# Optimization experiments

Hardware: AMD Instinct MI355X
Metric: run time of the kernel (lower is better)

The kernel has to match this reference:

```python
import jax, jax.numpy as jnp
import numpy as np

HEADS = 4
DIM_HEAD = 32
GROUPS = 32  # min(256//4, 32)
EPS = 1e-5


def setup_inputs() -> dict:
    key = jax.random.key(0)
    ks = jax.random.split(key, 6)
    B, C, H, W = 16, 256, 64, 64
    hidden = HEADS * DIM_HEAD  # 128
    return {
        "x": jax.random.normal(ks[0], (B, C, H, W), dtype=jnp.float32),
        "gn_w": jax.random.uniform(ks[1], (C,), dtype=jnp.float32),
        "gn_b": jax.random.normal(ks[2], (C,), dtype=jnp.float32) * 0.05,
        "qkv_w": jax.random.normal(ks[3], (3 * hidden, C), dtype=jnp.float32) * 0.05,
        "qkv_b": jax.random.normal(ks[4], (3 * hidden,), dtype=jnp.float32) * 0.05,
        "out_w": jax.random.normal(ks[5], (C, hidden), dtype=jnp.float32) * 0.05,
        "out_b": jnp.zeros((C,), dtype=jnp.float32),
    }


def _forward_single(x, gn_w, gn_b, qkv_w, qkv_b, out_w, out_b):
    # x: (c, h, w)
    c, h, w = x.shape
    # GroupNorm over (channels-in-group, h, w)
    xg = x.reshape(GROUPS, c // GROUPS, h, w)
    mean = xg.mean(axis=(1, 2, 3), keepdims=True)
    var = xg.var(axis=(1, 2, 3), keepdims=True)
    xn = ((xg - mean) * jax.lax.rsqrt(var + EPS)).reshape(c, h, w)
    xn = xn * gn_w[:, None, None] + gn_b[:, None, None]
    # 1x1 conv QKV projection
    qkv = jnp.einsum('oc,chw->ohw', qkv_w, xn) + qkv_b[:, None, None]
    qkv = qkv.reshape(3, HEADS, DIM_HEAD, h * w)
    q, k, v = qkv[0], qkv[1], qkv[2]
    k = jax.nn.softmax(k, axis=-1)  # softmax over spatial
    context = jnp.einsum('hdn,hen->hde', k, v)   # (heads, d, d)
    out = jnp.einsum('hde,hdn->hen', context, q)  # (heads, d, n)
    out = out.reshape(HEADS * DIM_HEAD, h, w)
    # 1x1 conv output projection
    return jnp.einsum('oc,chw->ohw', out_w, out) + out_b[:, None, None]


def reference(x, gn_w, gn_b, qkv_w, qkv_b, out_w, out_b):
    f = lambda xi: _forward_single(xi, gn_w, gn_b, qkv_w, qkv_b, out_w, out_b)
    return jax.vmap(f)(x)
```

## Files before the change

kernel.cpp:

```cpp
#include <hip/hip_runtime.h>
#include <stdint.h>

typedef unsigned short u16;
typedef __attribute__((ext_vector_type(8))) short bf16x8;
typedef __attribute__((ext_vector_type(4))) float f32x4;

#define B_   16
#define C_   256
#define HW_  4096
#define QR_  384
#define HID_ 128

__device__ __forceinline__ float b2f(u16 u) {
  union { uint32_t i; float f; } v; v.i = ((uint32_t)u) << 16; return v.f;
}
__device__ __forceinline__ u16 f2b(float f) {
  union { float f; uint32_t i; } v; v.f = f;
  uint32_t r = (v.i + 0x7FFFu + ((v.i >> 16) & 1u)) >> 16;
  return (u16)r;
}

__global__ __launch_bounds__(256) void gn_stats_conv_kernel(
    const float* __restrict__ x, const float* __restrict__ gnw,
    const float* __restrict__ gnb, float* __restrict__ scale,
    float* __restrict__ shiftv,
    const float* __restrict__ qkvw, u16* __restrict__ cqkvw,
    u16* __restrict__ wqT)
{
  if (blockIdx.x >= 512) {
    int bi = blockIdx.x - 512;
    int t = threadIdx.x;
    if (bi < 96) {
      int i = bi * 256 + t;
      float4 f = ((const float4*)qkvw)[i];
      ushort4 o;
      o.x = f2b(f.x); o.y = f2b(f.y); o.z = f2b(f.z); o.w = f2b(f.w);
      ((ushort4*)cqkvw)[i] = o;
      return;
    }
    __shared__ u16 tl[16][272];
    for (int j = 0; j < 8; ++j) {
      int d = j * 16 + (t >> 4);
      int cb = (t & 15) * 16;
#pragma unroll
      for (int ii = 0; ii < 16; ++ii)
        tl[t >> 4][cb + ii] = f2b(qkvw[(size_t)d * 256 + cb + ii]);
      __syncthreads();
      union { u16 v[16]; uint4 q[2]; } pk;
#pragma unroll
      for (int dd = 0; dd < 16; ++dd) pk.v[dd] = tl[dd][t];
      *(uint4*)(wqT + (size_t)t * 128 + j * 16)     = pk.q[0];
      *(uint4*)(wqT + (size_t)t * 128 + j * 16 + 8) = pk.q[1];
      __syncthreads();
    }
    return;
  }
  int b = blockIdx.x >> 5, g = blockIdx.x & 31;
  const float* p = x + ((size_t)b * C_ + g * 8) * HW_;
  int t = threadIdx.x;
  float s = 0.f, sq = 0.f;
#pragma unroll
  for (int i = 0; i < 16; ++i) {
    float4 u0 = *(const float4*)(p + t * 8 + i * 2048);
    float4 u1 = *(const float4*)(p + t * 8 + i * 2048 + 4);
    s  += u0.x + u0.y + u0.z + u0.w + u1.x + u1.y + u1.z + u1.w;
    sq += u0.x*u0.x + u0.y*u0.y + u0.z*u0.z + u0.w*u0.w
        + u1.x*u1.x + u1.y*u1.y + u1.z*u1.z + u1.w*u1.w;
  }
#pragma unroll
  for (int off = 32; off > 0; off >>= 1) {
    s  += __shfl_down(s, off);
    sq += __shfl_down(sq, off);
  }
  __shared__ float ps[4], pq[4], mr[2];
  int lane = t & 63, w = t >> 6;
  if (lane == 0) { ps[w] = s; pq[w] = sq; }
  __syncthreads();
  if (t == 0) {
    float S = ps[0] + ps[1] + ps[2] + ps[3];
    float Q = pq[0] + pq[1] + pq[2] + pq[3];
    float mean = S * (1.f / 32768.f);
    float var  = Q * (1.f / 32768.f) - mean * mean;
    mr[0] = mean; mr[1] = rsqrtf(var + 1e-5f);
  }
  __syncthreads();
  if (t < 8) {
    int c = g * 8 + t;
    float sc = gnw[c] * mr[1];
    scale[b * C_ + c]  = sc;
    shiftv[b * C_ + c] = gnb[c] - mr[0] * sc;
  }
}

__global__ __launch_bounds__(256) void gn_transpose_kernel(
    const float* __restrict__ x, u16* __restrict__ dst,
    const float* __restrict__ scale, const float* __restrict__ shiftv)
{
  int nt = blockIdx.x, ct = blockIdx.y, b = blockIdx.z;
  const float* S = x + (size_t)b * C_ * HW_;
  u16* D = dst + (size_t)b * HW_ * C_;
  __shared__ __align__(16) u16 tile[64][136];
  int t = threadIdx.x;
  int n0 = nt * 128, c0 = ct * 64;
  int r = t >> 2, seg = (t & 3) * 32;
  float sc = scale[(size_t)b * C_ + c0 + r];
  float sh = shiftv[(size_t)b * C_ + c0 + r];
#pragma unroll
  for (int i = 0; i < 4; ++i) {
    const float* rp = S + (size_t)(c0 + r) * HW_ + n0 + seg + i * 8;
    float4 u0 = *(const float4*)(rp);
    float4 u1 = *(const float4*)(rp + 4);
    float f[8] = {u0.x, u0.y, u0.z, u0.w, u1.x, u1.y, u1.z, u1.w};
    uint4 o;
    uint32_t* op = (uint32_t*)&o;
#pragma unroll
    for (int j = 0; j < 4; ++j) {
      op[j] = (uint32_t)f2b(f[2 * j] * sc + sh)
            | ((uint32_t)f2b(f[2 * j + 1] * sc + sh) << 16);
    }
    *(uint4*)&tile[r][seg + i * 8] = o;
  }
  __syncthreads();
#pragma unroll
  for (int i = 0; i < 4; ++i) {
    int m = t * 4 + i;
    int n_l = m >> 3, cg = (m & 7) * 8;
    union { u16 v[8]; uint4 q; } pk;
#pragma unroll
    for (int e = 0; e < 8; ++e) pk.v[e] = tile[cg + e][n_l];
    *(uint4*)(D + (size_t)(n0 + n_l) * C_ + c0 + cg) = pk.q;
  }
}

__global__ __launch_bounds__(512) void kv_ctx_kernel(
    const u16* __restrict__ A,
    const u16* __restrict__ Bt,
    float* __restrict__ ctx_part,
    float* __restrict__ s_part)
{
  const int K = C_;
  int nt = blockIdx.x, b = blockIdx.y;
  const u16* Ab = A;
  const u16* Bb = Bt + (size_t)b * HW_ * C_ + (size_t)nt * 128 * K;
  __shared__ __align__(16) union {
    struct { u16 lA[256 * 64]; u16 lB[128 * 64]; } st;
    struct { u16 ek[128][136]; u16 vv[128][136]; float sred[2][128]; } ep;
    float cred[4096];
  } sm;
  int t = threadIdx.x;
  int lane = t & 63, w = t >> 6;
  int quad = lane >> 4, l16 = lane & 15;
  int wm = (w >> 1) * 64, wn = (w & 1) * 64;
  f32x4 acc[4][4];
#pragma unroll
  for (int i = 0; i < 4; ++i)
#pragma unroll
    for (int j = 0; j < 4; ++j)
#pragma unroll
      for (int r = 0; r < 4; ++r) acc[i][j][r] = 0.f;

  for (int k0 = 0; k0 < K; k0 += 64) {
    __syncthreads();
#pragma unroll
    for (int q = 0; q < 4; ++q) {
      int ch = q * 512 + t;
      int row = ch >> 3, off = (ch & 7) * 8;
      __builtin_amdgcn_global_load_lds(
          (const __attribute__((address_space(1))) void*)(Ab + (size_t)row * K + k0 + off),
          (__attribute__((address_space(3))) void*)(sm.st.lA + ch * 8), 16, 0, 0);
    }
#pragma unroll
    for (int q = 0; q < 2; ++q) {
      int ch = q * 512 + t;
      int row = ch >> 3, off = (ch & 7) * 8;
      __builtin_amdgcn_global_load_lds(
          (const __attribute__((address_space(1))) void*)(Bb + (size_t)row * K + k0 + off),
          (__attribute__((address_space(3))) void*)(sm.st.lB + ch * 8), 16, 0, 0);
    }
    __syncthreads();
    const bf16x8* A8 = (const bf16x8*)sm.st.lA;
    const bf16x8* B8 = (const bf16x8*)sm.st.lB;
#pragma unroll
    for (int kk = 0; kk < 2; ++kk) {
      bf16x8 af[4], bfr[4];
#pragma unroll
      for (int i = 0; i < 4; ++i) af[i]  = A8[(wm + i * 16 + l16) * 8 + kk * 4 + quad];
#pragma unroll
      for (int j = 0; j < 4; ++j) bfr[j] = B8[(wn + j * 16 + l16) * 8 + kk * 4 + quad];
#pragma unroll
      for (int i = 0; i < 4; ++i)
#pragma unroll
        for (int j = 0; j < 4; ++j)
          acc[i][j] = __builtin_amdgcn_mfma_f32_16x16x32_bf16(af[i], bfr[j],
                                                              acc[i][j], 0, 0, 0);
    }
  }

  __syncthreads();
  int h = w >> 1, nh = w & 1;
  if (w < 4) {
    float sl[4][4];
#pragma unroll
    for (int i = 0; i < 4; ++i)
#pragma unroll
      for (int r = 0; r < 4; ++r) sl[i][r] = 0.f;
#pragma unroll
    for (int i = 0; i < 4; ++i)
#pragma unroll
      for (int j = 0; j < 4; ++j)
#pragma unroll
        for (int r = 0; r < 4; ++r) {
          float e = __expf(acc[i][j][r]);
          sl[i][r] += e;
          sm.ep.ek[wm + i * 16 + quad * 4 + r][wn + j * 16 + l16] = f2b(e);
        }
#pragma unroll
    for (int i = 0; i < 4; ++i)
#pragma unroll
      for (int r = 0; r < 4; ++r) {
        float v = sl[i][r];
        v += __shfl_xor(v, 1);
        v += __shfl_xor(v, 2);
        v += __shfl_xor(v, 4);
        v += __shfl_xor(v, 8);
        if (l16 == 0) sm.ep.sred[nh][wm + i * 16 + quad * 4 + r] = v;
      }
  } else {
#pragma unroll
    for (int i = 0; i < 4; ++i)
#pragma unroll
      for (int j = 0; j < 4; ++j)
#pragma unroll
        for (int r = 0; r < 4; ++r)
          sm.ep.vv[wm - 128 + i * 16 + quad * 4 + r][wn + j * 16 + l16] =
              f2b(acc[i][j][r]);
  }
  __syncthreads();
  if (t < 128)
    s_part[((size_t)b * 32 + nt) * 128 + t] = sm.ep.sred[0][t] + sm.ep.sred[1][t];

  f32x4 c2[2][2];
#pragma unroll
  for (int i = 0; i < 2; ++i)
#pragma unroll
    for (int j = 0; j < 2; ++j)
#pragma unroll
      for (int r = 0; r < 4; ++r) c2[i][j][r] = 0.f;
#pragma unroll
  for (int kk = 0; kk < 2; ++kk) {
    bf16x8 ae[2], be[2];
#pragma unroll
    for (int i = 0; i < 2; ++i)
      ae[i] = *(const bf16x8*)&sm.ep.ek[h * 32 + i * 16 + l16][nh * 64 + kk * 32 + quad * 8];
#pragma unroll
    for (int j = 0; j < 2; ++j)
      be[j] = *(const bf16x8*)&sm.ep.vv[h * 32 + j * 16 + l16][nh * 64 + kk * 32 + quad * 8];
#pragma unroll
    for (int i = 0; i < 2; ++i)
#pragma unroll
      for (int j = 0; j < 2; ++j)
        c2[i][j] = __builtin_amdgcn_mfma_f32_16x16x32_bf16(ae[i], be[j], c2[i][j], 0, 0, 0);
  }
  __syncthreads();
  if (nh == 0) {
#pragma unroll
    for (int i = 0; i < 2; ++i)
#pragma unroll
      for (int j = 0; j < 2; ++j)
#pragma unroll
        for (int r = 0; r < 4; ++r)
          sm.cred[h * 1024 + (i * 16 + quad * 4 + r) * 32 + j * 16 + l16] = c2[i][j][r];
  }
  __syncthreads();
  if (nh == 1) {
#pragma unroll
    for (int i = 0; i < 2; ++i)
#pragma unroll
      for (int j = 0; j < 2; ++j)
#pragma unroll
        for (int r = 0; r < 4; ++r)
          sm.cred[h * 1024 + (i * 16 + quad * 4 + r) * 32 + j * 16 + l16] += c2[i][j][r];
  }
  __syncthreads();
  float4* dst = (float4*)(ctx_part + ((size_t)b * 32 + nt) * 4096);
  const float4* src4 = (const float4*)sm.cred;
  dst[t] = src4[t];
  dst[t + 512] = src4[t + 512];
}

__global__ __launch_bounds__(256) void fold_kernel(
    const float* __restrict__ ctx_part, const float* __restrict__ s_part,
    const float* __restrict__ outw, const float* __restrict__ qkvb,
    u16* __restrict__ wf, float* __restrict__ btp)
{
  int b = blockIdx.x >> 2, h = blockIdx.x & 3;
  int t = threadIdx.x;
  __shared__ float cs[1024];
  __shared__ float sinv[32];
  const float* cp = ctx_part + ((size_t)b * 32) * 4096 + h * 1024;
  float4 aa = make_float4(0.f, 0.f, 0.f, 0.f);
  for (int ntb = 0; ntb < 32; ++ntb) {
    float4 v = *(const float4*)(cp + (size_t)ntb * 4096 + t * 4);
    aa.x += v.x; aa.y += v.y; aa.z += v.z; aa.w += v.w;
  }
  *(float4*)&cs[t * 4] = aa;
  if (t < 32) {
    float ssum = 0.f;
    for (int ntb = 0; ntb < 32; ++ntb)
      ssum += s_part[((size_t)b * 32 + ntb) * 128 + h * 32 + t];
    sinv[t] = 1.f / ssum;
  }
  __syncthreads();
  int o = t;
  const float* wr = outw + (size_t)o * HID_ + h * 32;
  float wv[32];
  float cb = 0.f;
#pragma unroll
  for (int e = 0; e < 32; ++e) {
    wv[e] = wr[e];
    cb += wv[e] * qkvb[256 + h * 32 + e];
  }
  union { u16 v[32]; uint4 q[4]; } pk;
  float bacc = 0.f;
#pragma unroll
  for (int d = 0; d < 32; ++d) {
    float a = 0.f;
#pragma unroll
    for (int e = 0; e < 32; ++e) a += wv[e] * cs[d * 32 + e];
    float val = a * sinv[d] + cb;
    pk.v[d] = f2b(val);
    bacc += val * qkvb[h * 32 + d];
  }
  uint4* dp = (uint4*)(wf + ((size_t)b * C_ + o) * HID_ + h * 32);
#pragma unroll
  for (int i = 0; i < 4; ++i) dp[i] = pk.q[i];
  btp[((size_t)b * 4 + h) * 256 + o] = bacc;
}

__global__ __launch_bounds__(256) void wtot_gemm_kernel(
    const u16* __restrict__ wfp, const u16* __restrict__ wqT,
    u16* __restrict__ wtot)
{
  const int K = HID_;
  int nt = blockIdx.x, mt = blockIdx.y, b = blockIdx.z;
  const u16* Ab = wfp + (size_t)b * C_ * HID_ + (size_t)mt * 128 * K;
  const u16* Bb = wqT + (size_t)nt * 128 * K;
  __shared__ __align__(16) u16 lA[128 * 64];
  __shared__ __align__(16) u16 lB[128 * 64];
  int t = threadIdx.x;
  int lane = t & 63, w = t >> 6;
  int quad = lane >> 4, l16 = lane & 15;
  int wm = (w >> 1) * 64, wn = (w & 1) * 64;
  f32x4 acc[4][4];
#pragma unroll
  for (int i = 0; i < 4; ++i)
#pragma unroll
    for (int j = 0; j < 4; ++j)
#pragma unroll
      for (int r = 0; r < 4; ++r) acc[i][j][r] = 0.f;

  for (int k0 = 0; k0 < K; k0 += 64) {
    __syncthreads();
#pragma unroll
    for (int q = 0; q < 4; ++q) {
      int ch = q * 256 + t;
      int row = ch >> 3, off = (ch & 7) * 8;
      __builtin_amdgcn_global_load_lds(
          (const __attribute__((address_space(1))) void*)(Ab + (size_t)row * K + k0 + off),
          (__attribute__((address_space(3))) void*)(lA + ch * 8), 16, 0, 0);
      __builtin_amdgcn_global_load_lds(
          (const __attribute__((address_space(1))) void*)(Bb + (size_t)row * K + k0 + off),
          (__attribute__((address_space(3))) void*)(lB + ch * 8), 16, 0, 0);
    }
    __syncthreads();
    const bf16x8* A8 = (const bf16x8*)lA;
    const bf16x8* B8 = (const bf16x8*)lB;
#pragma unroll
    for (int kk = 0; kk < 2; ++kk) {
      bf16x8 af[4], bfr[4];
#pragma unroll
      for (int i = 0; i < 4; ++i) af[i]  = A8[(wm + i * 16 + l16) * 8 + kk * 4 + quad];
#pragma unroll
      for (int j = 0; j < 4; ++j) bfr[j] = B8[(wn + j * 16 + l16) * 8 + kk * 4 + quad];
#pragma unroll
      for (int i = 0; i < 4; ++i)
#pragma unroll
        for (int j = 0; j < 4; ++j)
          acc[i][j] = __builtin_amdgcn_mfma_f32_16x16x32_bf16(af[i], bfr[j],
                                                              acc[i][j], 0, 0, 0);
    }
  }
  u16* Wb = wtot + (size_t)b * C_ * C_;
#pragma unroll
  for (int i = 0; i < 4; ++i) {
#pragma unroll
    for (int rg = 0; rg < 4; ++rg) {
      int o = mt * 128 + wm + i * 16 + quad * 4 + rg;
#pragma unroll
      for (int j = 0; j < 4; ++j) {
        int c = nt * 128 + wn + j * 16 + l16;
        Wb[(size_t)o * C_ + c] = f2b(acc[i][j][rg]);
      }
    }
  }
}

__global__ __launch_bounds__(256) void out_gemm_kernel(
    const u16* __restrict__ wtot, const u16* __restrict__ Bt,
    const float* __restrict__ outb, const float* __restrict__ btp,
    float* __restrict__ Cout)
{
  const int K = C_;
  int nt = blockIdx.x, mt = blockIdx.y, b = blockIdx.z;
  const u16* Ab = wtot + (size_t)b * C_ * C_ + (size_t)mt * 128 * K;
  const u16* Bb = Bt + (size_t)b * HW_ * C_ + (size_t)nt * 128 * K;
  __shared__ __align__(16) u16 lA[128 * 64];
  __shared__ __align__(16) u16 lB[128 * 64];
  int t = threadIdx.x;
  int lane = t & 63, w = t >> 6;
  int quad = lane >> 4, l16 = lane & 15;
  int wm = (w >> 1) * 64, wn = (w & 1) * 64;
  f32x4 acc[4][4];
#pragma unroll
  for (int i = 0; i < 4; ++i)
#pragma unroll
    for (int j = 0; j < 4; ++j)
#pragma unroll
      for (int r = 0; r < 4; ++r) acc[i][j][r] = 0.f;

  for (int k0 = 0; k0 < K; k0 += 64) {
    __syncthreads();
#pragma unroll
    for (int q = 0; q < 4; ++q) {
      int ch = q * 256 + t;
      int row = ch >> 3, off = (ch & 7) * 8;
      __builtin_amdgcn_global_load_lds(
          (const __attribute__((address_space(1))) void*)(Ab + (size_t)row * K + k0 + off),
          (__attribute__((address_space(3))) void*)(lA + ch * 8), 16, 0, 0);
      __builtin_amdgcn_global_load_lds(
          (const __attribute__((address_space(1))) void*)(Bb + (size_t)row * K + k0 + off),
          (__attribute__((address_space(3))) void*)(lB + ch * 8), 16, 0, 0);
    }
    __syncthreads();
    const bf16x8* A8 = (const bf16x8*)lA;
    const bf16x8* B8 = (const bf16x8*)lB;
#pragma unroll
    for (int kk = 0; kk < 2; ++kk) {
      bf16x8 af[4], bfr[4];
#pragma unroll
      for (int i = 0; i < 4; ++i) af[i]  = A8[(wm + i * 16 + l16) * 8 + kk * 4 + quad];
#pragma unroll
      for (int j = 0; j < 4; ++j) bfr[j] = B8[(wn + j * 16 + l16) * 8 + kk * 4 + quad];
#pragma unroll
      for (int i = 0; i < 4; ++i)
#pragma unroll
        for (int j = 0; j < 4; ++j)
          acc[i][j] = __builtin_amdgcn_mfma_f32_16x16x32_bf16(af[i], bfr[j],
                                                              acc[i][j], 0, 0, 0);
    }
  }
#pragma unroll
  for (int i = 0; i < 4; ++i) {
#pragma unroll
    for (int rg = 0; rg < 4; ++rg) {
      int o = mt * 128 + wm + i * 16 + quad * 4 + rg;
      float bsv = outb[o]
                + btp[((size_t)b * 4 + 0) * 256 + o]
                + btp[((size_t)b * 4 + 1) * 256 + o]
                + btp[((size_t)b * 4 + 2) * 256 + o]
                + btp[((size_t)b * 4 + 3) * 256 + o];
      size_t rowbase = (size_t)b * C_ * HW_ + (size_t)o * HW_;
#pragma unroll
      for (int j = 0; j < 4; ++j) {
        int n = nt * 128 + wn + j * 16 + l16;
        Cout[rowbase + n] = acc[i][j][rg] + bsv;
      }
    }
  }
}

extern "C" void kernel_launch(void* const* d_in, const int* in_sizes, int n_in,
                              void* d_out, int out_size, void* d_ws, size_t ws_size,
                              hipStream_t stream)
{
  const float* x    = (const float*)d_in[0];
  const float* gnw  = (const float*)d_in[1];
  const float* gnb  = (const float*)d_in[2];
  const float* qkvw = (const float*)d_in[3];
  const float* qkvb = (const float*)d_in[4];
  const float* outw = (const float*)d_in[5];
  const float* outb = (const float*)d_in[6];

  char* p = (char*)d_ws;
  float* scale  = (float*)p;            p += (size_t)B_ * C_ * 4;
  float* shiftv = (float*)p;            p += (size_t)B_ * C_ * 4;
  u16* cqkvw = (u16*)p;                 p += (size_t)QR_ * C_ * 2;
  u16* wqT   = (u16*)p;                 p += (size_t)C_ * HID_ * 2;
  u16* xn_t  = (u16*)p;                 p += (size_t)B_ * HW_ * C_ * 2;
  u16* wf    = (u16*)p;                 p += (size_t)B_ * C_ * HID_ * 2;
  u16* wtot  = (u16*)p;                 p += (size_t)B_ * C_ * C_ * 2;
  float* ctxp = (float*)p;              p += (size_t)B_ * 32 * 4 * 1024 * 4;
  float* sp   = (float*)p;              p += (size_t)B_ * 32 * 128 * 4;
  float* btp  = (float*)p;

  gn_stats_conv_kernel<<<609, 256, 0, stream>>>(x, gnw, gnb, scale, shiftv,
                                                qkvw, cqkvw, wqT);
  gn_transpose_kernel<<<dim3(32, 4, 16), 256, 0, stream>>>(x, xn_t, scale, shiftv);
  kv_ctx_kernel<<<dim3(32, 16), 512, 0, stream>>>(cqkvw + 128 * C_, xn_t, ctxp, sp);
  fold_kernel<<<64, 256, 0, stream>>>(ctxp, sp, outw, qkvb, wf, btp);
  wtot_gemm_kernel<<<dim3(2, 2, 16), 256, 0, stream>>>(wf, wqT, wtot);
  out_gemm_kernel<<<dim3(32, 2, 16), 256, 0, stream>>>(wtot, xn_t, outb, btp,
                                                       (float*)d_out);
}
```

Measured before the change: 195.1 us.

## Fuse fold and wtot GEMM via last-block atomic counter; vectorize output stores

The separate wtot GEMM kernel is merged into the fold kernel. The last of the four head-blocks per batch, detected with an atomic counter and threadfence, stages the folded weights in LDS, computes the combined bias and the 256x256 wtot product with MFMA, and writes packed bf16. This removes one kernel launch and the btp partial-bias round trip. The output GEMM swaps its MFMA operand order so that each lane holds four consecutive spatial outputs and can write them as float4. The cost is that only 16 blocks do the wtot work, so that step runs with little parallelism.

```diff
diff --git a/kernel.cpp b/kernel.cpp
--- a/kernel.cpp
+++ b/kernel.cpp
@@ -25,7 +25,7 @@
     const float* __restrict__ gnb, float* __restrict__ scale,
     float* __restrict__ shiftv,
     const float* __restrict__ qkvw, u16* __restrict__ cqkvw,
-    u16* __restrict__ wqT)
+    u16* __restrict__ wqT, unsigned int* __restrict__ cnt)
 {
   if (blockIdx.x >= 512) {
     int bi = blockIdx.x - 512;
@@ -38,6 +38,7 @@
       ((ushort4*)cqkvw)[i] = o;
       return;
     }
+    if (t < 16) cnt[t] = 0;
     __shared__ u16 tl[16][272];
     for (int j = 0; j < 8; ++j) {
       int d = j * 16 + (t >> 4);
@@ -288,15 +289,19 @@
   dst[t + 512] = src4[t + 512];
 }
 
-__global__ __launch_bounds__(256) void fold_kernel(
+__global__ __launch_bounds__(256) void foldwtot_kernel(
     const float* __restrict__ ctx_part, const float* __restrict__ s_part,
     const float* __restrict__ outw, const float* __restrict__ qkvb,
-    u16* __restrict__ wf, float* __restrict__ btp)
+    const u16* __restrict__ wqT, const float* __restrict__ outb,
+    u16* __restrict__ wf, u16* __restrict__ wtot,
+    float* __restrict__ btot, unsigned int* __restrict__ cnt)
 {
   int b = blockIdx.x >> 2, h = blockIdx.x & 3;
   int t = threadIdx.x;
   __shared__ float cs[1024];
   __shared__ float sinv[32];
+  __shared__ unsigned int oldc;
+  __shared__ __align__(16) u16 wfl[256 * 136];
   const float* cp = ctx_part + ((size_t)b * 32) * 4096 + h * 1024;
   float4 aa = make_float4(0.f, 0.f, 0.f, 0.f);
   for (int ntb = 0; ntb < 32; ++ntb) {
@@ -311,104 +316,82 @@
     sinv[t] = 1.f / ssum;
   }
   __syncthreads();
-  int o = t;
-  const float* wr = outw + (size_t)o * HID_ + h * 32;
-  float wv[32];
-  float cb = 0.f;
-#pragma unroll
-  for (int e = 0; e < 32; ++e) {
-    wv[e] = wr[e];
-    cb += wv[e] * qkvb[256 + h * 32 + e];
-  }
-  union { u16 v[32]; uint4 q[4]; } pk;
-  float bacc = 0.f;
-#pragma unroll
-  for (int d = 0; d < 32; ++d) {
-    float a = 0.f;
-#pragma unroll
-    for (int e = 0; e < 32; ++e) a += wv[e] * cs[d * 32 + e];
-    float val = a * sinv[d] + cb;
-    pk.v[d] = f2b(val);
-    bacc += val * qkvb[h * 32 + d];
-  }
-  uint4* dp = (uint4*)(wf + ((size_t)b * C_ + o) * HID_ + h * 32);
-#pragma unroll
-  for (int i = 0; i < 4; ++i) dp[i] = pk.q[i];
-  btp[((size_t)b * 4 + h) * 256 + o] = bacc;
-}
-
-__global__ __launch_bounds__(256) void wtot_gemm_kernel(
-    const u16* __restrict__ wfp, const u16* __restrict__ wqT,
-    u16* __restrict__ wtot)
-{
-  const int K = HID_;
-  int nt = blockIdx.x, mt = blockIdx.y, b = blockIdx.z;
-  const u16* Ab = wfp + (size_t)b * C_ * HID_ + (size_t)mt * 128 * K;
-  const u16* Bb = wqT + (size_t)nt * 128 * K;
-  __shared__ __align__(16) u16 lA[128 * 64];
-  __shared__ __align__(16) u16 lB[128 * 64];
-  int t = threadIdx.x;
+  {
+    int o = t;
+    const float* wr = outw + (size_t)o * HID_ + h * 32;
+    float wv[32];
+    float cb = 0.f;
+#pragma unroll
+    for (int e = 0; e < 32; ++e) {
+      wv[e] = wr[e];
+      cb += wv[e] * qkvb[256 + h * 32 + e];
+    }
+    union { u16 v[32]; uint4 q[4]; } pk;
+#pragma unroll
+    for (int d = 0; d < 32; ++d) {
+      float a = 0.f;
+#pragma unroll
+      for (int e = 0; e < 32; ++e) a += wv[e] * cs[d * 32 + e];
+      pk.v[d] = f2b(a * sinv[d] + cb);
+    }
+    uint4* dp = (uint4*)(wf + ((size_t)b * C_ + o) * HID_ + h * 32);
+#pragma unroll
+    for (int i = 0; i < 4; ++i) dp[i] = pk.q[i];
+  }
+
+  __threadfence();
+  __syncthreads();
+  if (t == 0) oldc = atomicAdd(&cnt[b], 1u);
+  __syncthreads();
+  if (oldc != 3) return;
+  __threadfence();
+
+  const uint4* ws4 = (const uint4*)(wf + (size_t)b * C_ * HID_);
+  for (int i = t; i < 4096; i += 256) {
+    uint4 v = ws4[i];
+    int o_ = i >> 4, off = (i & 15) * 8;
+    *(uint4*)&wfl[o_ * 136 + off] = v;
+  }
+  __syncthreads();
+  {
+    float a = outb[t];
+#pragma unroll
+    for (int d = 0; d < 128; ++d) a += b2f(wfl[t * 136 + d]) * qkvb[d];
+    btot[(size_t)b * C_ + t] = a;
+  }
   int lane = t & 63, w = t >> 6;
   int quad = lane >> 4, l16 = lane & 15;
-  int wm = (w >> 1) * 64, wn = (w & 1) * 64;
-  f32x4 acc[4][4];
-#pragma unroll
-  for (int i = 0; i < 4; ++i)
-#pragma unroll
-    for (int j = 0; j < 4; ++j)
-#pragma unroll
-      for (int r = 0; r < 4; ++r) acc[i][j][r] = 0.f;
-
-  for (int k0 = 0; k0 < K; k0 += 64) {
-    __syncthreads();
-#pragma unroll
-    for (int q = 0; q < 4; ++q) {
-      int ch = q * 256 + t;
-      int row = ch >> 3, off = (ch & 7) * 8;
-      __builtin_amdgcn_global_load_lds(
-          (const __attribute__((address_space(1))) void*)(Ab + (size_t)row * K + k0 + off),
-          (__attribute__((address_space(3))) void*)(lA + ch * 8), 16, 0, 0);
-      __builtin_amdgcn_global_load_lds(
-          (const __attribute__((address_space(1))) void*)(Bb + (size_t)row * K + k0 + off),
-          (__attribute__((address_space(3))) void*)(lB + ch * 8), 16, 0, 0);
-    }
-    __syncthreads();
-    const bf16x8* A8 = (const bf16x8*)lA;
-    const bf16x8* B8 = (const bf16x8*)lB;
-#pragma unroll
-    for (int kk = 0; kk < 2; ++kk) {
-      bf16x8 af[4], bfr[4];
-#pragma unroll
-      for (int i = 0; i < 4; ++i) af[i]  = A8[(wm + i * 16 + l16) * 8 + kk * 4 + quad];
-#pragma unroll
-      for (int j = 0; j < 4; ++j) bfr[j] = B8[(wn + j * 16 + l16) * 8 + kk * 4 + quad];
-#pragma unroll
-      for (int i = 0; i < 4; ++i)
-#pragma unroll
-        for (int j = 0; j < 4; ++j)
-          acc[i][j] = __builtin_amdgcn_mfma_f32_16x16x32_bf16(af[i], bfr[j],
-                                                              acc[i][j], 0, 0, 0);
-    }
-  }
   u16* Wb = wtot + (size_t)b * C_ * C_;
-#pragma unroll
-  for (int i = 0; i < 4; ++i) {
-#pragma unroll
-    for (int rg = 0; rg < 4; ++rg) {
-      int o = mt * 128 + wm + i * 16 + quad * 4 + rg;
-#pragma unroll
-      for (int j = 0; j < 4; ++j) {
-        int c = nt * 128 + wn + j * 16 + l16;
-        Wb[(size_t)o * C_ + c] = f2b(acc[i][j][rg]);
+  for (int j = 0; j < 16; ++j) {
+    f32x4 a4[4];
+#pragma unroll
+    for (int i = 0; i < 4; ++i)
+#pragma unroll
+      for (int r = 0; r < 4; ++r) a4[i][r] = 0.f;
+#pragma unroll
+    for (int kk = 0; kk < 4; ++kk) {
+      bf16x8 bfj = *(const bf16x8*)(wqT + (size_t)(j * 16 + l16) * 128 + kk * 32 + quad * 8);
+#pragma unroll
+      for (int i = 0; i < 4; ++i) {
+        bf16x8 afi = *(const bf16x8*)&wfl[(w * 64 + i * 16 + l16) * 136 + kk * 32 + quad * 8];
+        a4[i] = __builtin_amdgcn_mfma_f32_16x16x32_bf16(bfj, afi, a4[i], 0, 0, 0);
       }
+    }
+#pragma unroll
+    for (int i = 0; i < 4; ++i) {
+      int oo = w * 64 + i * 16 + l16;
+      int c0 = j * 16 + quad * 4;
+      uint2 p2;
+      p2.x = (uint32_t)f2b(a4[i][0]) | ((uint32_t)f2b(a4[i][1]) << 16);
+      p2.y = (uint32_t)f2b(a4[i][2]) | ((uint32_t)f2b(a4[i][3]) << 16);
+      *(uint2*)(Wb + (size_t)oo * C_ + c0) = p2;
     }
   }
 }
 
 __global__ __launch_bounds__(256) void out_gemm_kernel(
     const u16* __restrict__ wtot, const u16* __restrict__ Bt,
-    const float* __restrict__ outb, const float* __restrict__ btp,
-    float* __restrict__ Cout)
+    const float* __restrict__ btot, float* __restrict__ Cout)
 {
   const int K = C_;
   int nt = blockIdx.x, mt = blockIdx.y, b = blockIdx.z;
@@ -422,11 +405,11 @@
   int wm = (w >> 1) * 64, wn = (w & 1) * 64;
   f32x4 acc[4][4];
 #pragma unroll
-  for (int i = 0; i < 4; ++i)
-#pragma unroll
-    for (int j = 0; j < 4; ++j)
-#pragma unroll
-      for (int r = 0; r < 4; ++r) acc[i][j][r] = 0.f;
+  for (int j = 0; j < 4; ++j)
+#pragma unroll
+    for (int i = 0; i < 4; ++i)
+#pragma unroll
+      for (int r = 0; r < 4; ++r) acc[j][i][r] = 0.f;
 
   for (int k0 = 0; k0 < K; k0 += 64) {
     __syncthreads();
@@ -452,29 +435,24 @@
 #pragma unroll
       for (int j = 0; j < 4; ++j) bfr[j] = B8[(wn + j * 16 + l16) * 8 + kk * 4 + quad];
 #pragma unroll
-      for (int i = 0; i < 4; ++i)
-#pragma unroll
-        for (int j = 0; j < 4; ++j)
-          acc[i][j] = __builtin_amdgcn_mfma_f32_16x16x32_bf16(af[i], bfr[j],
-                                                              acc[i][j], 0, 0, 0);
+      for (int j = 0; j < 4; ++j)
+#pragma unroll
+        for (int i = 0; i < 4; ++i)
+          acc[j][i] = __builtin_amdgcn_mfma_f32_16x16x32_bf16(bfr[j], af[i],
+                                                              acc[j][i], 0, 0, 0);
     }
   }
 #pragma unroll
   for (int i = 0; i < 4; ++i) {
-#pragma unroll
-    for (int rg = 0; rg < 4; ++rg) {
-      int o = mt * 128 + wm + i * 16 + quad * 4 + rg;
-      float bsv = outb[o]
-                + btp[((size_t)b * 4 + 0) * 256 + o]
-                + btp[((size_t)b * 4 + 1) * 256 + o]
-                + btp[((size_t)b * 4 + 2) * 256 + o]
-                + btp[((size_t)b * 4 + 3) * 256 + o];
-      size_t rowbase = (size_t)b * C_ * HW_ + (size_t)o * HW_;
-#pragma unroll
-      for (int j = 0; j < 4; ++j) {
-        int n = nt * 128 + wn + j * 16 + l16;
-        Cout[rowbase + n] = acc[i][j][rg] + bsv;
-      }
+    int o = mt * 128 + wm + i * 16 + l16;
+    float bo = btot[(size_t)b * C_ + o];
+    size_t rowbase = (size_t)b * C_ * HW_ + (size_t)o * HW_;
+#pragma unroll
+    for (int j = 0; j < 4; ++j) {
+      int n0 = nt * 128 + wn + j * 16 + quad * 4;
+      float4 v = make_float4(acc[j][i][0] + bo, acc[j][i][1] + bo,
+                             acc[j][i][2] + bo, acc[j][i][3] + bo);
+      *(float4*)(Cout + rowbase + n0) = v;
     }
   }
 }
@@ -501,14 +479,15 @@
   u16* wtot  = (u16*)p;                 p += (size_t)B_ * C_ * C_ * 2;
   float* ctxp = (float*)p;              p += (size_t)B_ * 32 * 4 * 1024 * 4;
   float* sp   = (float*)p;              p += (size_t)B_ * 32 * 128 * 4;
-  float* btp  = (float*)p;
+  float* btot = (float*)p;              p += (size_t)B_ * C_ * 4;
+  unsigned int* cnt = (unsigned int*)p; p += 16 * 4;
 
   gn_stats_conv_kernel<<<609, 256, 0, stream>>>(x, gnw, gnb, scale, shiftv,
-                                                qkvw, cqkvw, wqT);
+                                                qkvw, cqkvw, wqT, cnt);
   gn_transpose_kernel<<<dim3(32, 4, 16), 256, 0, stream>>>(x, xn_t, scale, shiftv);
   kv_ctx_kernel<<<dim3(32, 16), 512, 0, stream>>>(cqkvw + 128 * C_, xn_t, ctxp, sp);
-  fold_kernel<<<64, 256, 0, stream>>>(ctxp, sp, outw, qkvb, wf, btp);
-  wtot_gemm_kernel<<<dim3(2, 2, 16), 256, 0, stream>>>(wf, wqT, wtot);
-  out_gemm_kernel<<<dim3(32, 2, 16), 256, 0, stream>>>(wtot, xn_t, outb, btp,
+  foldwtot_kernel<<<64, 256, 0, stream>>>(ctxp, sp, outw, qkvb, wqT, outb,
+                                          wf, wtot, btot, cnt);
+  out_gemm_kernel<<<dim3(32, 2, 16), 256, 0, stream>>>(wtot, xn_t, btot,
                                                        (float*)d_out);
 }
```

Result: slower. 222.0 us (+13.8%).

## Atomic context reduction, MFMA fold kernel, and vectorized output stores

Applied to the files above, without the earlier changes.

kv_ctx now accumulates per-batch context and softmax sums directly with float atomics into a buffer that extra blocks of the first kernel zero, instead of writing 32 partials per batch. The fold kernel no longer reduces those partials and becomes an MFMA-based bf16 matmul with shuffle reductions for the bias term. The output GEMM swaps MFMA operand order so each lane holds four consecutive spatial outputs, allowing float4 stores. These changes target partial-buffer traffic, the scalar fold loop and scattered scalar stores, at the cost of atomic contention and summation order that varies between runs.

```diff
diff --git a/kernel.cpp b/kernel.cpp
--- a/kernel.cpp
+++ b/kernel.cpp
@@ -25,7 +25,7 @@
     const float* __restrict__ gnb, float* __restrict__ scale,
     float* __restrict__ shiftv,
     const float* __restrict__ qkvw, u16* __restrict__ cqkvw,
-    u16* __restrict__ wqT)
+    u16* __restrict__ wqT, float* __restrict__ ctxs)
 {
   if (blockIdx.x >= 512) {
     int bi = blockIdx.x - 512;
@@ -38,6 +38,11 @@
       ((ushort4*)cqkvw)[i] = o;
       return;
     }
+    if (bi >= 97) {
+      int z = (bi - 97) * 256 + t;
+      ((float4*)ctxs)[z] = make_float4(0.f, 0.f, 0.f, 0.f);
+      return;
+    }
     __shared__ u16 tl[16][272];
     for (int j = 0; j < 8; ++j) {
       int d = j * 16 + (t >> 4);
@@ -135,8 +140,8 @@
 __global__ __launch_bounds__(512) void kv_ctx_kernel(
     const u16* __restrict__ A,
     const u16* __restrict__ Bt,
-    float* __restrict__ ctx_part,
-    float* __restrict__ s_part)
+    float* __restrict__ ctx,
+    float* __restrict__ sv)
 {
   const int K = C_;
   int nt = blockIdx.x, b = blockIdx.y;
@@ -237,7 +242,7 @@
   }
   __syncthreads();
   if (t < 128)
-    s_part[((size_t)b * 32 + nt) * 128 + t] = sm.ep.sred[0][t] + sm.ep.sred[1][t];
+    atomicAdd(&sv[(size_t)b * 128 + t], sm.ep.sred[0][t] + sm.ep.sred[1][t]);
 
   f32x4 c2[2][2];
 #pragma unroll
@@ -282,59 +287,95 @@
           sm.cred[h * 1024 + (i * 16 + quad * 4 + r) * 32 + j * 16 + l16] += c2[i][j][r];
   }
   __syncthreads();
-  float4* dst = (float4*)(ctx_part + ((size_t)b * 32 + nt) * 4096);
-  const float4* src4 = (const float4*)sm.cred;
-  dst[t] = src4[t];
-  dst[t + 512] = src4[t + 512];
-}
-
-__global__ __launch_bounds__(256) void fold_kernel(
-    const float* __restrict__ ctx_part, const float* __restrict__ s_part,
+  float* ctxb = ctx + (size_t)b * 4096;
+#pragma unroll
+  for (int u = 0; u < 8; ++u)
+    atomicAdd(&ctxb[t + u * 512], sm.cred[t + u * 512]);
+}
+
+__global__ __launch_bounds__(256) void fold_mfma_kernel(
+    const float* __restrict__ ctx, const float* __restrict__ sv,
     const float* __restrict__ outw, const float* __restrict__ qkvb,
     u16* __restrict__ wf, float* __restrict__ btp)
 {
   int b = blockIdx.x >> 2, h = blockIdx.x & 3;
   int t = threadIdx.x;
-  __shared__ float cs[1024];
-  __shared__ float sinv[32];
-  const float* cp = ctx_part + ((size_t)b * 32) * 4096 + h * 1024;
-  float4 aa = make_float4(0.f, 0.f, 0.f, 0.f);
-  for (int ntb = 0; ntb < 32; ++ntb) {
-    float4 v = *(const float4*)(cp + (size_t)ntb * 4096 + t * 4);
-    aa.x += v.x; aa.y += v.y; aa.z += v.z; aa.w += v.w;
-  }
-  *(float4*)&cs[t * 4] = aa;
-  if (t < 32) {
-    float ssum = 0.f;
-    for (int ntb = 0; ntb < 32; ++ntb)
-      ssum += s_part[((size_t)b * 32 + ntb) * 128 + h * 32 + t];
-    sinv[t] = 1.f / ssum;
-  }
-  __syncthreads();
-  int o = t;
-  const float* wr = outw + (size_t)o * HID_ + h * 32;
-  float wv[32];
-  float cb = 0.f;
-#pragma unroll
-  for (int e = 0; e < 32; ++e) {
-    wv[e] = wr[e];
-    cb += wv[e] * qkvb[256 + h * 32 + e];
-  }
-  union { u16 v[32]; uint4 q[4]; } pk;
-  float bacc = 0.f;
-#pragma unroll
-  for (int d = 0; d < 32; ++d) {
-    float a = 0.f;
-#pragma unroll
-    for (int e = 0; e < 32; ++e) a += wv[e] * cs[d * 32 + e];
-    float val = a * sinv[d] + cb;
-    pk.v[d] = f2b(val);
-    bacc += val * qkvb[h * 32 + d];
-  }
-  uint4* dp = (uint4*)(wf + ((size_t)b * C_ + o) * HID_ + h * 32);
-#pragma unroll
-  for (int i = 0; i < 4; ++i) dp[i] = pk.q[i];
-  btp[((size_t)b * 4 + h) * 256 + o] = bacc;
+  int lane = t & 63, w = t >> 6;
+  int quad = lane >> 4, l16 = lane & 15;
+  __shared__ __align__(16) u16 wfl[256][40];
+
+  float bv8[8];
+#pragma unroll
+  for (int e = 0; e < 8; ++e) bv8[e] = qkvb[256 + h * 32 + quad * 8 + e];
+
+  bf16x8 bf[2];
+#pragma unroll
+  for (int j = 0; j < 2; ++j) {
+    int d = j * 16 + l16;
+    float si = 1.f / sv[(size_t)b * 128 + h * 32 + d];
+    const float* cp = ctx + (size_t)b * 4096 + h * 1024 + d * 32 + quad * 8;
+    float4 c0 = *(const float4*)(cp);
+    float4 c1 = *(const float4*)(cp + 4);
+    float cv[8] = {c0.x, c0.y, c0.z, c0.w, c1.x, c1.y, c1.z, c1.w};
+    u16* bp = (u16*)&bf[j];
+#pragma unroll
+    for (int e = 0; e < 8; ++e) bp[e] = f2b(cv[e] * si + bv8[e]);
+  }
+
+  f32x4 acc[4][2];
+#pragma unroll
+  for (int i = 0; i < 4; ++i) {
+    int o = w * 64 + i * 16 + l16;
+    const float* ap = outw + (size_t)o * HID_ + h * 32 + quad * 8;
+    float4 a0 = *(const float4*)(ap);
+    float4 a1 = *(const float4*)(ap + 4);
+    float av[8] = {a0.x, a0.y, a0.z, a0.w, a1.x, a1.y, a1.z, a1.w};
+    bf16x8 af;
+    u16* app = (u16*)&af;
+#pragma unroll
+    for (int e = 0; e < 8; ++e) app[e] = f2b(av[e]);
+    f32x4 z;
+#pragma unroll
+    for (int r = 0; r < 4; ++r) z[r] = 0.f;
+#pragma unroll
+    for (int j = 0; j < 2; ++j)
+      acc[i][j] = __builtin_amdgcn_mfma_f32_16x16x32_bf16(af, bf[j], z, 0, 0, 0);
+  }
+
+  float bqv[2];
+#pragma unroll
+  for (int j = 0; j < 2; ++j) bqv[j] = qkvb[h * 32 + j * 16 + l16];
+#pragma unroll
+  for (int i = 0; i < 4; ++i) {
+#pragma unroll
+    for (int r = 0; r < 4; ++r) {
+      float v = acc[i][0][r] * bqv[0] + acc[i][1][r] * bqv[1];
+      v += __shfl_xor(v, 1);
+      v += __shfl_xor(v, 2);
+      v += __shfl_xor(v, 4);
+      v += __shfl_xor(v, 8);
+      if (l16 == 0) {
+        int o = w * 64 + i * 16 + quad * 4 + r;
+        btp[((size_t)b * 4 + h) * 256 + o] = v;
+      }
+    }
+  }
+
+#pragma unroll
+  for (int i = 0; i < 4; ++i)
+#pragma unroll
+    for (int j = 0; j < 2; ++j)
+#pragma unroll
+      for (int r = 0; r < 4; ++r)
+        wfl[w * 64 + i * 16 + quad * 4 + r][j * 16 + l16] = f2b(acc[i][j][r]);
+  __syncthreads();
+  int rr = t >> 2, rof = (t & 3) * 8;
+#pragma unroll
+  for (int it = 0; it < 4; ++it) {
+    int o = it * 64 + rr;
+    *(uint4*)(wf + ((size_t)b * C_ + o) * HID_ + h * 32 + rof) =
+        *(const uint4*)&wfl[o][rof];
+  }
 }
 
 __global__ __launch_bounds__(256) void wtot_gemm_kernel(
@@ -422,11 +463,11 @@
   int wm = (w >> 1) * 64, wn = (w & 1) * 64;
   f32x4 acc[4][4];
 #pragma unroll
-  for (int i = 0; i < 4; ++i)
-#pragma unroll
-    for (int j = 0; j < 4; ++j)
-#pragma unroll
-      for (int r = 0; r < 4; ++r) acc[i][j][r] = 0.f;
+  for (int j = 0; j < 4; ++j)
+#pragma unroll
+    for (int i = 0; i < 4; ++i)
+#pragma unroll
+      for (int r = 0; r < 4; ++r) acc[j][i][r] = 0.f;
 
   for (int k0 = 0; k0 < K; k0 += 64) {
     __syncthreads();
@@ -452,29 +493,28 @@
 #pragma unroll
       for (int j = 0; j < 4; ++j) bfr[j] = B8[(wn + j * 16 + l16) * 8 + kk * 4 + quad];
 #pragma unroll
-      for (int i = 0; i < 4; ++i)
-#pragma unroll
-        for (int j = 0; j < 4; ++j)
-          acc[i][j] = __builtin_amdgcn_mfma_f32_16x16x32_bf16(af[i], bfr[j],
-                                                              acc[i][j], 0, 0, 0);
+      for (int j = 0; j < 4; ++j)
+#pragma unroll
+        for (int i = 0; i < 4; ++i)
+          acc[j][i] = __builtin_amdgcn_mfma_f32_16x16x32_bf16(bfr[j], af[i],
+                                                              acc[j][i], 0, 0, 0);
     }
   }
 #pragma unroll
   for (int i = 0; i < 4; ++i) {
-#pragma unroll
-    for (int rg = 0; rg < 4; ++rg) {
-      int o = mt * 128 + wm + i * 16 + quad * 4 + rg;
-      float bsv = outb[o]
-                + btp[((size_t)b * 4 + 0) * 256 + o]
-                + btp[((size_t)b * 4 + 1) * 256 + o]
-                + btp[((size_t)b * 4 + 2) * 256 + o]
-                + btp[((size_t)b * 4 + 3) * 256 + o];
-      size_t rowbase = (size_t)b * C_ * HW_ + (size_t)o * HW_;
-#pragma unroll
-      for (int j = 0; j < 4; ++j) {
-        int n = nt * 128 + wn + j * 16 + l16;
-        Cout[rowbase + n] = acc[i][j][rg] + bsv;
-      }
+    int o = mt * 128 + wm + i * 16 + l16;
+    float bo = outb[o]
+             + btp[((size_t)b * 4 + 0) * 256 + o]
+             + btp[((size_t)b * 4 + 1) * 256 + o]
+             + btp[((size_t)b * 4 + 2) * 256 + o]
+             + btp[((size_t)b * 4 + 3) * 256 + o];
+    size_t rowbase = (size_t)b * C_ * HW_ + (size_t)o * HW_;
+#pragma unroll
+    for (int j = 0; j < 4; ++j) {
+      int n0 = nt * 128 + wn + j * 16 + quad * 4;
+      float4 v = make_float4(acc[j][i][0] + bo, acc[j][i][1] + bo,
+                             acc[j][i][2] + bo, acc[j][i][3] + bo);
+      *(float4*)(Cout + rowbase + n0) = v;
     }
   }
 }
@@ -499,15 +539,16 @@
   u16* xn_t  = (u16*)p;                 p += (size_t)B_ * HW_ * C_ * 2;
   u16* wf    = (u16*)p;                 p += (size_t)B_ * C_ * HID_ * 2;
   u16* wtot  = (u16*)p;                 p += (size_t)B_ * C_ * C_ * 2;
-  float* ctxp = (float*)p;              p += (size_t)B_ * 32 * 4 * 1024 * 4;
-  float* sp   = (float*)p;              p += (size_t)B_ * 32 * 128 * 4;
+  float* ctxs = (float*)p;              p += (size_t)67584 * 4;
   float* btp  = (float*)p;
-
-  gn_stats_conv_kernel<<<609, 256, 0, stream>>>(x, gnw, gnb, scale, shiftv,
-                                                qkvw, cqkvw, wqT);
+  float* ctx = ctxs;
+  float* sv  = ctxs + 65536;
+
+  gn_stats_conv_kernel<<<675, 256, 0, stream>>>(x, gnw, gnb, scale, shiftv,
+                                                qkvw, cqkvw, wqT, ctxs);
   gn_transpose_kernel<<<dim3(32, 4, 16), 256, 0, stream>>>(x, xn_t, scale, shiftv);
-  kv_ctx_kernel<<<dim3(32, 16), 512, 0, stream>>>(cqkvw + 128 * C_, xn_t, ctxp, sp);
-  fold_kernel<<<64, 256, 0, stream>>>(ctxp, sp, outw, qkvb, wf, btp);
+  kv_ctx_kernel<<<dim3(32, 16), 512, 0, stream>>>(cqkvw + 128 * C_, xn_t, ctx, sv);
+  fold_mfma_kernel<<<64, 256, 0, stream>>>(ctx, sv, outw, qkvb, wf, btp);
   wtot_gemm_kernel<<<dim3(2, 2, 16), 256, 0, stream>>>(wf, wqT, wtot);
   out_gemm_kernel<<<dim3(32, 2, 16), 256, 0, stream>>>(wtot, xn_t, outb, btp,
                                                        (float*)d_out);
```

After: 195.0 us. No clear change (-0.1%).
